# Performance work log

Hardware: AMD Instinct MI355X
Metric: run time of the kernel (lower is better)

Reference implementation:

```python
import jax, jax.numpy as jnp
import numpy as np

N, D = 8192, 128

def setup_inputs() -> dict:
    key = jax.random.key(0)
    kF, kS = jax.random.split(key)
    F = jax.random.normal(kF, (N, D), dtype=jnp.float32)
    S = jax.random.uniform(kS, (N, N), dtype=jnp.float32)
    return {"F": F, "S": S, "t": 1, "T": 10}

def reference(F, S, t, T):
    # Pairwise squared euclidean distances via Gram trick:
    # D_ij = ||f_i||^2 + ||f_j||^2 - 2 f_i . f_j  (same math as norm(F[:,None]-F)^2)
    sq = jnp.sum(F * F, axis=1)                      # [N]
    dist2 = sq[:, None] + sq[None, :] - 2.0 * (F @ F.T)  # [N, N]
    # select=False: loss = sum over i of sum_j dist2[i,j] * S[i,j]
    loss = jnp.sum(dist2 * S)
    return loss
```

## Files before the change

### kernel.cpp

```cpp
#include <hip/hip_runtime.h>

#define NN 8192
#define DD 128
#define BI 128
#define BJ 64
#define GX (NN / BJ)
#define GY (NN / BI)
#define NBLK (GX * GY)

typedef __attribute__((ext_vector_type(8))) short bf16x8;
typedef __attribute__((ext_vector_type(4))) float f32x4;

__device__ __forceinline__ ushort f2bf(float x) {
    unsigned u = __float_as_uint(x);
    unsigned r = u + 0x7FFFu + ((u >> 16) & 1u);
    return (ushort)(r >> 16);
}

__device__ __forceinline__ void async16(void* lds, const void* g) {
    __builtin_amdgcn_global_load_lds(
        (const __attribute__((address_space(1))) unsigned*)g,
        (__attribute__((address_space(3))) unsigned*)lds, 16, 0, 0);
}

__global__ void prep_kernel(const float* __restrict__ F, ushort* __restrict__ Fbf,
                            float* __restrict__ sq, int doFbf) {
    int gtid = blockIdx.x * blockDim.x + threadIdx.x;
    int row  = gtid >> 6;
    int lane = threadIdx.x & 63;
    const float2 v = *(const float2*)(F + (size_t)row * DD + lane * 2);
    if (doFbf)
        ((ushort2*)(Fbf + (size_t)row * DD))[lane] = make_ushort2(f2bf(v.x), f2bf(v.y));
    float s = v.x * v.x + v.y * v.y;
    #pragma unroll
    for (int off = 32; off > 0; off >>= 1) s += __shfl_down(s, off);
    if (lane == 0) sq[row] = s;
}

__global__ __launch_bounds__(256, 4) void tile_kernel(
        const ushort* __restrict__ Fbf, const float* __restrict__ S,
        const float* __restrict__ sq, float* __restrict__ partials) {
    __shared__ ushort lI[BI * DD];
    __shared__ float  red[4];

    const int gi  = blockIdx.y * BI;
    const int gj  = blockIdx.x * BJ;
    const int tid = threadIdx.x;
    const int w = tid >> 6, l = tid & 63;
    const int fr = l & 15, g = l >> 4;
    const int jw = w * 16;

    #pragma unroll
    for (int it = 0; it < 8; ++it) {
        const int c   = it * 4 + w;
        const int row = c * 4 + (l >> 4);
        const int src = ((l & 15) * 16) ^ ((row & 7) << 4);
        async16((char*)lI + c * 1024, (const char*)(Fbf + (size_t)(gi + row) * DD) + src);
    }

    bf16x8 af[4];
    #pragma unroll
    for (int kk = 0; kk < 4; ++kk)
        af[kk] = *(const bf16x8*)(Fbf + (size_t)(gj + jw + fr) * DD + kk * 32 + g * 8);
    float si[8];
    #pragma unroll
    for (int ct = 0; ct < 8; ++ct) si[ct] = sq[gi + ct * 16 + fr];
    const float4 sjv = *(const float4*)(sq + gj + jw + g * 4);

    __syncthreads();

    f32x4 sv[8];
    const float* sb = S + (size_t)(gi + fr) * NN + gj + jw + g * 4;
    #pragma unroll
    for (int ct = 0; ct < 8; ++ct)
        sv[ct] = *(const f32x4*)(sb + (size_t)ct * 16 * NN);
    __builtin_amdgcn_sched_barrier(0);

    f32x4 acc[8];
    #pragma unroll
    for (int ct = 0; ct < 8; ++ct) acc[ct] = (f32x4){0.f, 0.f, 0.f, 0.f};
    #pragma unroll
    for (int ct = 0; ct < 8; ++ct) {
        const int row = ct * 16 + fr;
        const int sw  = (row & 7) << 4;
        #pragma unroll
        for (int kk = 0; kk < 4; ++kk) {
            const bf16x8 bfr = *(const bf16x8*)((const char*)lI + row * 256 +
                                                ((kk * 64 + g * 16) ^ sw));
            acc[ct] = __builtin_amdgcn_mfma_f32_16x16x32_bf16(af[kk], bfr, acc[ct], 0, 0, 0);
        }
    }

    float part0 = 0.f, part1 = 0.f;
    #pragma unroll
    for (int ct = 0; ct < 8; ++ct) {
        const f32x4 s4 = sv[ct];
        const float sic = si[ct];
        part0 += s4.x * ((sic + sjv.x) - 2.f * acc[ct][0]);
        part1 += s4.y * ((sic + sjv.y) - 2.f * acc[ct][1]);
        part0 += s4.z * ((sic + sjv.z) - 2.f * acc[ct][2]);
        part1 += s4.w * ((sic + sjv.w) - 2.f * acc[ct][3]);
    }
    float part = part0 + part1;

    #pragma unroll
    for (int off = 32; off > 0; off >>= 1) part += __shfl_down(part, off);
    if (l == 0) red[w] = part;
    __syncthreads();
    if (tid == 0)
        partials[blockIdx.y * gridDim.x + blockIdx.x] =
            (red[0] + red[1]) + (red[2] + red[3]);
}

__global__ __launch_bounds__(256, 2) void tile_fb_kernel(
        const float* __restrict__ F, const float* __restrict__ S,
        const float* __restrict__ sq, float* __restrict__ partials) {
    __shared__ ushort lI[BI * DD];
    __shared__ ushort lJ[BI * DD];
    __shared__ float  sqi[BI];
    __shared__ float  sqj[BI];
    __shared__ float  red[4];

    const int gi = blockIdx.y * BI, gj = blockIdx.x * BI;
    const int tid = threadIdx.x;
    const int w = tid >> 6, l = tid & 63;

    const int r0 = tid >> 5;
    const int c4 = (tid & 31) * 4;
    #pragma unroll
    for (int it = 0; it < 16; ++it) {
        const int row = it * 8 + r0;
        const float4 va = *(const float4*)(F + (size_t)(gi + row) * DD + c4);
        const float4 vb = *(const float4*)(F + (size_t)(gj + row) * DD + c4);
        int byte = row * 256 + c4 * 2;
        byte ^= (row & 7) << 4;
        *(ushort4*)((char*)lI + byte) =
            make_ushort4(f2bf(va.x), f2bf(va.y), f2bf(va.z), f2bf(va.w));
        *(ushort4*)((char*)lJ + byte) =
            make_ushort4(f2bf(vb.x), f2bf(vb.y), f2bf(vb.z), f2bf(vb.w));
    }
    if (tid < 128) sqi[tid] = sq[gi + tid];
    else           sqj[tid - 128] = sq[gj + tid - 128];
    __syncthreads();

    const int fr = l & 15;
    const int g  = l >> 4;
    const int jw = w * 32;

    float4 sv0[8], sv1[8];
    #pragma unroll
    for (int ct = 0; ct < 8; ++ct) {
        const float* srow = S + (size_t)(gi + ct * 16 + fr) * NN + gj + jw + g * 4;
        sv0[ct] = *(const float4*)(srow);
        sv1[ct] = *(const float4*)(srow + 16);
    }

    bf16x8 afrag[2][4];
    #pragma unroll
    for (int kk = 0; kk < 4; ++kk) {
        int row = jw + fr;
        int byte = row * 256 + kk * 64 + g * 16; byte ^= (row & 7) << 4;
        afrag[0][kk] = *(const bf16x8*)((const char*)lJ + byte);
        row = jw + 16 + fr;
        byte = row * 256 + kk * 64 + g * 16; byte ^= (row & 7) << 4;
        afrag[1][kk] = *(const bf16x8*)((const char*)lJ + byte);
    }

    f32x4 acc[2][8];
    #pragma unroll
    for (int ct = 0; ct < 8; ++ct) {
        acc[0][ct] = (f32x4){0.f, 0.f, 0.f, 0.f};
        acc[1][ct] = (f32x4){0.f, 0.f, 0.f, 0.f};
    }
    #pragma unroll
    for (int ct = 0; ct < 8; ++ct) {
        #pragma unroll
        for (int kk = 0; kk < 4; ++kk) {
            const int row = ct * 16 + fr;
            int byte = row * 256 + kk * 64 + g * 16; byte ^= (row & 7) << 4;
            const bf16x8 bfrag = *(const bf16x8*)((const char*)lI + byte);
            acc[0][ct] = __builtin_amdgcn_mfma_f32_16x16x32_bf16(afrag[0][kk], bfrag, acc[0][ct], 0, 0, 0);
            acc[1][ct] = __builtin_amdgcn_mfma_f32_16x16x32_bf16(afrag[1][kk], bfrag, acc[1][ct], 0, 0, 0);
        }
    }

    const float4 sj0 = *(const float4*)(sqj + jw + g * 4);
    const float4 sj1 = *(const float4*)(sqj + jw + 16 + g * 4);
    float part = 0.f;
    #pragma unroll
    for (int ct = 0; ct < 8; ++ct) {
        const float sic = sqi[ct * 16 + fr];
        const float4 s0 = sv0[ct], s1 = sv1[ct];
        part += s0.x * (sic + sj0.x - 2.f * acc[0][ct][0]);
        part += s0.y * (sic + sj0.y - 2.f * acc[0][ct][1]);
        part += s0.z * (sic + sj0.z - 2.f * acc[0][ct][2]);
        part += s0.w * (sic + sj0.w - 2.f * acc[0][ct][3]);
        part += s1.x * (sic + sj1.x - 2.f * acc[1][ct][0]);
        part += s1.y * (sic + sj1.y - 2.f * acc[1][ct][1]);
        part += s1.z * (sic + sj1.z - 2.f * acc[1][ct][2]);
        part += s1.w * (sic + sj1.w - 2.f * acc[1][ct][3]);
    }

    #pragma unroll
    for (int off = 32; off > 0; off >>= 1) part += __shfl_down(part, off);
    if (l == 0) red[w] = part;
    __syncthreads();
    if (tid == 0)
        partials[blockIdx.y * gridDim.x + blockIdx.x] = (red[0] + red[1]) + (red[2] + red[3]);
}

__global__ void reduce_kernel(const float* __restrict__ partials, float* __restrict__ out, int n) {
    __shared__ float sm[256];
    const int t = threadIdx.x;
    float s = 0.f;
    for (int i = t; i < n; i += 256) s += partials[i];
    sm[t] = s;
    __syncthreads();
    for (int off = 128; off > 0; off >>= 1) {
        if (t < off) sm[t] += sm[t + off];
        __syncthreads();
    }
    if (t == 0) out[0] = sm[0];
}

extern "C" void kernel_launch(void* const* d_in, const int* in_sizes, int n_in,
                              void* d_out, int out_size, void* d_ws, size_t ws_size,
                              hipStream_t stream) {
    const float* F = (const float*)d_in[0];
    const float* S = (const float*)d_in[1];
    float* sq        = (float*)d_ws;
    float* partials  = sq + NN;
    ushort* Fbf      = (ushort*)((char*)d_ws + 128 * 1024);
    float* out       = (float*)d_out;

    const size_t need = 128 * 1024 + (size_t)NN * DD * 2 + 256;
    const int fast = (ws_size >= need) ? 1 : 0;

    prep_kernel<<<NN / 4, 256, 0, stream>>>(F, Fbf, sq, fast);
    if (fast) {
        tile_kernel<<<dim3(GX, GY), 256, 0, stream>>>(Fbf, S, sq, partials);
        reduce_kernel<<<1, 256, 0, stream>>>(partials, out, NBLK);
    } else {
        tile_fb_kernel<<<dim3(GY, GY), 256, 0, stream>>>(F, S, sq, partials);
        reduce_kernel<<<1, 256, 0, stream>>>(partials, out, GY * GY);
    }
}
```

Baseline: 76.72 us.

## Use 128x128 tiles with 512 threads and stage both operand tiles in LDS

```diff
diff --git a/kernel.cpp b/kernel.cpp
--- a/kernel.cpp
+++ b/kernel.cpp
@@ -2,11 +2,8 @@
 
 #define NN 8192
 #define DD 128
-#define BI 128
-#define BJ 64
-#define GX (NN / BJ)
-#define GY (NN / BI)
-#define NBLK (GX * GY)
+#define BM 128
+#define NTILE (NN / BM)
 
 typedef __attribute__((ext_vector_type(8))) short bf16x8;
 typedef __attribute__((ext_vector_type(4))) float f32x4;
@@ -21,6 +18,11 @@
     __builtin_amdgcn_global_load_lds(
         (const __attribute__((address_space(1))) unsigned*)g,
         (__attribute__((address_space(3))) unsigned*)lds, 16, 0, 0);
+}
+__device__ __forceinline__ void async4(void* lds, const void* g) {
+    __builtin_amdgcn_global_load_lds(
+        (const __attribute__((address_space(1))) unsigned*)g,
+        (__attribute__((address_space(3))) unsigned*)lds, 4, 0, 0);
 }
 
 __global__ void prep_kernel(const float* __restrict__ F, ushort* __restrict__ Fbf,
@@ -37,37 +39,37 @@
     if (lane == 0) sq[row] = s;
 }
 
-__global__ __launch_bounds__(256, 4) void tile_kernel(
+__global__ __launch_bounds__(512, 4) void tile_kernel(
         const ushort* __restrict__ Fbf, const float* __restrict__ S,
         const float* __restrict__ sq, float* __restrict__ partials) {
-    __shared__ ushort lI[BI * DD];
-    __shared__ float  red[4];
-
-    const int gi  = blockIdx.y * BI;
-    const int gj  = blockIdx.x * BJ;
+    __shared__ ushort lI[BM * DD];
+    __shared__ ushort lJ[BM * DD];
+    __shared__ float  sqi[BM];
+    __shared__ float  sqj[BM];
+    __shared__ float  red[8];
+
+    const int gi = blockIdx.y * BM, gj = blockIdx.x * BM;
     const int tid = threadIdx.x;
     const int w = tid >> 6, l = tid & 63;
-    const int fr = l & 15, g = l >> 4;
+
+    #pragma unroll
+    for (int it = 0; it < 4; ++it) {
+        const int chunk = it * 8 + w;
+        const int row = chunk * 4 + (l >> 4);
+        const int src = ((l & 15) * 16) ^ ((row & 7) << 4);
+        async16((char*)lI + chunk * 1024, (const char*)(Fbf + (size_t)(gi + row) * DD) + src);
+        async16((char*)lJ + chunk * 1024, (const char*)(Fbf + (size_t)(gj + row) * DD) + src);
+    }
+    if (w < 4) {
+        float* dstb = (w < 2 ? sqi : sqj) + (w & 1) * 64;
+        const float* srcb = sq + (w < 2 ? gi : gj) + (w & 1) * 64 + l;
+        async4(dstb, srcb);
+    }
+    __syncthreads();
+
+    const int fr = l & 15;
+    const int g  = l >> 4;
     const int jw = w * 16;
-
-    #pragma unroll
-    for (int it = 0; it < 8; ++it) {
-        const int c   = it * 4 + w;
-        const int row = c * 4 + (l >> 4);
-        const int src = ((l & 15) * 16) ^ ((row & 7) << 4);
-        async16((char*)lI + c * 1024, (const char*)(Fbf + (size_t)(gi + row) * DD) + src);
-    }
-
-    bf16x8 af[4];
-    #pragma unroll
-    for (int kk = 0; kk < 4; ++kk)
-        af[kk] = *(const bf16x8*)(Fbf + (size_t)(gj + jw + fr) * DD + kk * 32 + g * 8);
-    float si[8];
-    #pragma unroll
-    for (int ct = 0; ct < 8; ++ct) si[ct] = sq[gi + ct * 16 + fr];
-    const float4 sjv = *(const float4*)(sq + gj + jw + g * 4);
-
-    __syncthreads();
 
     f32x4 sv[8];
     const float* sb = S + (size_t)(gi + fr) * NN + gj + jw + g * 4;
@@ -76,26 +78,37 @@
         sv[ct] = *(const f32x4*)(sb + (size_t)ct * 16 * NN);
     __builtin_amdgcn_sched_barrier(0);
 
+    bf16x8 afrag[4];
+    #pragma unroll
+    for (int kk = 0; kk < 4; ++kk) {
+        const int row = jw + fr;
+        int byte = row * 256 + kk * 64 + g * 16;
+        byte ^= (row & 7) << 4;
+        afrag[kk] = *(const bf16x8*)((const char*)lJ + byte);
+    }
+
     f32x4 acc[8];
     #pragma unroll
     for (int ct = 0; ct < 8; ++ct) acc[ct] = (f32x4){0.f, 0.f, 0.f, 0.f};
+
     #pragma unroll
     for (int ct = 0; ct < 8; ++ct) {
         const int row = ct * 16 + fr;
         const int sw  = (row & 7) << 4;
         #pragma unroll
         for (int kk = 0; kk < 4; ++kk) {
-            const bf16x8 bfr = *(const bf16x8*)((const char*)lI + row * 256 +
-                                                ((kk * 64 + g * 16) ^ sw));
-            acc[ct] = __builtin_amdgcn_mfma_f32_16x16x32_bf16(af[kk], bfr, acc[ct], 0, 0, 0);
+            const bf16x8 bfrag = *(const bf16x8*)((const char*)lI + row * 256 +
+                                                  ((kk * 64 + g * 16) ^ sw));
+            acc[ct] = __builtin_amdgcn_mfma_f32_16x16x32_bf16(afrag[kk], bfrag, acc[ct], 0, 0, 0);
         }
     }
 
+    const float4 sjv = *(const float4*)(sqj + jw + g * 4);
     float part0 = 0.f, part1 = 0.f;
     #pragma unroll
     for (int ct = 0; ct < 8; ++ct) {
+        const float sic = sqi[ct * 16 + fr];
         const f32x4 s4 = sv[ct];
-        const float sic = si[ct];
         part0 += s4.x * ((sic + sjv.x) - 2.f * acc[ct][0]);
         part1 += s4.y * ((sic + sjv.y) - 2.f * acc[ct][1]);
         part0 += s4.z * ((sic + sjv.z) - 2.f * acc[ct][2]);
@@ -109,19 +122,20 @@
     __syncthreads();
     if (tid == 0)
         partials[blockIdx.y * gridDim.x + blockIdx.x] =
-            (red[0] + red[1]) + (red[2] + red[3]);
+            ((red[0] + red[1]) + (red[2] + red[3])) +
+            ((red[4] + red[5]) + (red[6] + red[7]));
 }
 
 __global__ __launch_bounds__(256, 2) void tile_fb_kernel(
         const float* __restrict__ F, const float* __restrict__ S,
         const float* __restrict__ sq, float* __restrict__ partials) {
-    __shared__ ushort lI[BI * DD];
-    __shared__ ushort lJ[BI * DD];
-    __shared__ float  sqi[BI];
-    __shared__ float  sqj[BI];
+    __shared__ ushort lI[BM * DD];
+    __shared__ ushort lJ[BM * DD];
+    __shared__ float  sqi[BM];
+    __shared__ float  sqj[BM];
     __shared__ float  red[4];
 
-    const int gi = blockIdx.y * BI, gj = blockIdx.x * BI;
+    const int gi = blockIdx.y * BM, gj = blockIdx.x * BM;
     const int tid = threadIdx.x;
     const int w = tid >> 6, l = tid & 63;
 
@@ -209,11 +223,11 @@
         partials[blockIdx.y * gridDim.x + blockIdx.x] = (red[0] + red[1]) + (red[2] + red[3]);
 }
 
-__global__ void reduce_kernel(const float* __restrict__ partials, float* __restrict__ out, int n) {
+__global__ void reduce_kernel(const float* __restrict__ partials, float* __restrict__ out) {
     __shared__ float sm[256];
     const int t = threadIdx.x;
     float s = 0.f;
-    for (int i = t; i < n; i += 256) s += partials[i];
+    for (int i = t; i < NTILE * NTILE; i += 256) s += partials[i];
     sm[t] = s;
     __syncthreads();
     for (int off = 128; off > 0; off >>= 1) {
@@ -228,20 +242,19 @@
                               hipStream_t stream) {
     const float* F = (const float*)d_in[0];
     const float* S = (const float*)d_in[1];
-    float* sq        = (float*)d_ws;
-    float* partials  = sq + NN;
-    ushort* Fbf      = (ushort*)((char*)d_ws + 128 * 1024);
-    float* out       = (float*)d_out;
-
-    const size_t need = 128 * 1024 + (size_t)NN * DD * 2 + 256;
+    float* sq       = (float*)d_ws;
+    float* partials = sq + NN;
+    ushort* Fbf     = (ushort*)((char*)d_ws + 48 * 1024);
+    float* out      = (float*)d_out;
+
+    const size_t need = 48 * 1024 + (size_t)NN * DD * 2 + 256;
     const int fast = (ws_size >= need) ? 1 : 0;
 
     prep_kernel<<<NN / 4, 256, 0, stream>>>(F, Fbf, sq, fast);
-    if (fast) {
-        tile_kernel<<<dim3(GX, GY), 256, 0, stream>>>(Fbf, S, sq, partials);
-        reduce_kernel<<<1, 256, 0, stream>>>(partials, out, NBLK);
-    } else {
-        tile_fb_kernel<<<dim3(GY, GY), 256, 0, stream>>>(F, S, sq, partials);
-        reduce_kernel<<<1, 256, 0, stream>>>(partials, out, GY * GY);
-    }
-}
+    dim3 grid(NTILE, NTILE);
+    if (fast)
+        tile_kernel<<<grid, 512, 0, stream>>>(Fbf, S, sq, partials);
+    else
+        tile_fb_kernel<<<grid, 256, 0, stream>>>(F, S, sq, partials);
+    reduce_kernel<<<1, 256, 0, stream>>>(partials, out);
+}
```

After: 63.93 us (median of 2 runs). 1.2x faster.
